# Kernel optimization log

Measured on AMD Instinct MI355X. Metric: run time of the kernel, lower is better.

## Reference

```python
import jax, jax.numpy as jnp
import numpy as np
import math

B, S, H, NH = 2, 2048, 2048, 16
HD = H // NH  # 128


def _rope_tables(seq_len, dim, base=10000.0):
    inv_freq = 1.0 / (base ** (np.arange(0, dim, 2, dtype=np.float32) / dim))
    t = np.arange(seq_len, dtype=np.float32)
    freqs = np.outer(t, inv_freq)                      # [S, dim/2]
    emb = np.concatenate([freqs, freqs], axis=-1)      # [S, dim] (HF layout)
    return jnp.asarray(np.cos(emb)), jnp.asarray(np.sin(emb))


def setup_inputs() -> dict:
    key = jax.random.key(0)
    ks = jax.random.split(key, 6)
    sc = 1.0 / math.sqrt(H)
    cos, sin = _rope_tables(S, HD)
    return {
        "hidden_states": jax.random.normal(ks[0], (B, S, H), jnp.float32),
        "wq": jax.random.normal(ks[1], (H, H), jnp.float32) * sc,
        "wk": jax.random.normal(ks[2], (H, H), jnp.float32) * sc,
        "wv": jax.random.normal(ks[3], (H, H), jnp.float32) * sc,
        "wo": jax.random.normal(ks[4], (H, H), jnp.float32) * sc,
        "cos": cos,
        "sin": sin,
        "attention_mask": jnp.ones((B, S), jnp.float32),
        "position_ids": jnp.broadcast_to(jnp.arange(S, dtype=jnp.int64), (B, S)),
    }


def _rotate_half(x):
    x1, x2 = jnp.split(x, 2, axis=-1)
    return jnp.concatenate([-x2, x1], axis=-1)


def reference(hidden_states, wq, wk, wv, wo, cos, sin, attention_mask, position_ids):
    b, s, _ = hidden_states.shape
    # projections (torch Linear: x @ W^T)
    q = (hidden_states @ wq.T).reshape(b, s, NH, HD).transpose(0, 2, 1, 3)
    k = (hidden_states @ wk.T).reshape(b, s, NH, HD).transpose(0, 2, 1, 3)
    v = (hidden_states @ wv.T).reshape(b, s, NH, HD).transpose(0, 2, 1, 3)
    # RoPE (HF apply_rotary_pos_emb): gather tables at position_ids -> [b,1,s,hd]
    c = cos[position_ids][:, None, :, :]
    sn = sin[position_ids][:, None, :, :]
    q = q * c + _rotate_half(q) * sn
    k = k * c + _rotate_half(k) * sn
    # dense attention scores [b,h,q,k]
    scores = jnp.einsum("bhqd,bhkd->bhqk", q, k) / math.sqrt(HD)
    adder = (1.0 - attention_mask)[:, None, None, :] * -10000.0
    scores = scores + adder
    probs = jax.nn.softmax(scores.astype(jnp.float32), axis=-1).astype(q.dtype)
    attn = jnp.einsum("bhqk,bhkd->bhqd", probs, v)
    attn = attn.transpose(0, 2, 1, 3).reshape(b, s, H)
    return attn @ wo.T
```

## Files before the change

### kernel.cpp

```cpp
#include <hip/hip_runtime.h>
#include <hip/hip_bf16.h>

#define B_SZ 2
#define S_LEN 2048
#define H_DIM 2048
#define N_HEAD 16
#define HD 128

using bf16 = __hip_bfloat16;
using bf16x8 = __bf16 __attribute__((ext_vector_type(8)));
using floatx4 = float __attribute__((ext_vector_type(4)));

typedef unsigned int __attribute__((address_space(1))) as1_uint;
typedef unsigned int __attribute__((address_space(3))) as3_uint;

__device__ inline void async_load16(const void* g, void* l) {
  __builtin_amdgcn_global_load_lds((const as1_uint*)g, (as3_uint*)l, 16, 0, 0);
}

__device__ inline void store_out(float* p, float v) { *p = v; }
__device__ inline void store_out(bf16* p, float v) { *p = __float2bfloat16(v); }

__global__ __launch_bounds__(256) void cast_kernel(const float* __restrict__ in,
                                                   bf16* __restrict__ out, int n4) {
  int i = blockIdx.x * 256 + threadIdx.x;
  if (i >= n4) return;
  const float4 v = ((const float4*)in)[i];
  union { bf16 h[4]; uint2 u; } o;
  o.h[0] = __float2bfloat16(v.x);
  o.h[1] = __float2bfloat16(v.y);
  o.h[2] = __float2bfloat16(v.z);
  o.h[3] = __float2bfloat16(v.w);
  ((uint2*)out)[i] = o.u;
}

__global__ __launch_bounds__(256) void cast4_kernel(
    const float* __restrict__ a, const float* __restrict__ b,
    const float* __restrict__ c, const float* __restrict__ d,
    bf16* __restrict__ oa, bf16* __restrict__ ob,
    bf16* __restrict__ oc, bf16* __restrict__ od) {
  int i = blockIdx.x * 256 + threadIdx.x;
  int sel = i >> 20;
  int j = i & 0xFFFFF;
  const float* src = sel == 0 ? a : sel == 1 ? b : sel == 2 ? c : d;
  bf16* dst = sel == 0 ? oa : sel == 1 ? ob : sel == 2 ? oc : od;
  const float4 v = ((const float4*)src)[j];
  union { bf16 h[4]; uint2 u; } o;
  o.h[0] = __float2bfloat16(v.x);
  o.h[1] = __float2bfloat16(v.y);
  o.h[2] = __float2bfloat16(v.z);
  o.h[3] = __float2bfloat16(v.w);
  ((uint2*)dst)[j] = o.u;
}

template <typename OutT>
__global__ __launch_bounds__(256) void gemm_bt(const bf16* __restrict__ A,
                                               const bf16* __restrict__ B,
                                               OutT* __restrict__ C,
                                               int M, int N, int K) {
  __shared__ alignas(16) bf16 As[128 * 32];
  __shared__ alignas(16) bf16 Bs[128 * 32];
  const int tid = threadIdx.x;
  const int wave = tid >> 6;
  const int lane = tid & 63;
  const int quad = lane >> 4;
  const int l16 = lane & 15;
  const int m0 = blockIdx.x * 128;
  const int n0 = blockIdx.y * 128;
  const int wm = (wave >> 1) * 64;
  const int wn = (wave & 1) * 64;

  const bf16* Ag = A + (size_t)(m0 + (tid >> 2)) * K + (tid & 3) * 8;
  const bf16* Bg = B + (size_t)(n0 + (tid >> 2)) * K + (tid & 3) * 8;
  char* AsB = (char*)As + wave * 1024;
  char* BsB = (char*)Bs + wave * 1024;
  const size_t rowskip = (size_t)64 * K;

  floatx4 acc[4][4] = {};

  for (int k0 = 0; k0 < K; k0 += 32) {
    async_load16(Ag + k0, AsB);
    async_load16(Ag + rowskip + k0, AsB + 4096);
    async_load16(Bg + k0, BsB);
    async_load16(Bg + rowskip + k0, BsB + 4096);
    __syncthreads();

    bf16x8 af[4], bfr[4];
#pragma unroll
    for (int i = 0; i < 4; i++)
      af[i] = *(const bf16x8*)&As[(wm + i * 16 + l16) * 32 + quad * 8];
#pragma unroll
    for (int j = 0; j < 4; j++)
      bfr[j] = *(const bf16x8*)&Bs[(wn + j * 16 + l16) * 32 + quad * 8];
#pragma unroll
    for (int i = 0; i < 4; i++)
#pragma unroll
      for (int j = 0; j < 4; j++)
        acc[i][j] = __builtin_amdgcn_mfma_f32_16x16x32_bf16(af[i], bfr[j], acc[i][j], 0, 0, 0);
    __syncthreads();
  }

#pragma unroll
  for (int i = 0; i < 4; i++) {
    const int row = m0 + wm + i * 16 + quad * 4;
#pragma unroll
    for (int j = 0; j < 4; j++) {
      const int col = n0 + wn + j * 16 + l16;
#pragma unroll
      for (int r = 0; r < 4; r++)
        store_out(&C[(size_t)(row + r) * N + col], acc[i][j][r]);
    }
  }
}

__global__ __launch_bounds__(512, 2) void gemm_qk_rope256(
    const bf16* __restrict__ A, const bf16* __restrict__ B,
    bf16* __restrict__ C, const float* __restrict__ cosT,
    const float* __restrict__ sinT, const int* __restrict__ pos) {
  __shared__ alignas(16) char lds[131072];
  const int tid = threadIdx.x;
  const int wv = tid >> 6;
  const int lane = tid & 63;
  const int quad = lane >> 4;
  const int l16 = lane & 15;
  const int lrow = lane >> 3;
  const int scol = ((lane & 7) << 4) ^ (lrow << 4);

  const int id = blockIdx.x;
  const int swz = (id & 7) * 32 + (id >> 3);
  const int m0 = (swz >> 4) * 256;
  const int n0 = (swz & 15) * 256;
  const int wrow = (wv >> 1) * 64;
  const int wcol = (wv & 1) * 128;

  const char* Ag = (const char*)A + (size_t)(m0 + wv * 8 + lrow) * 4096 + scol;
  const char* Bg = (const char*)B + (size_t)(n0 + wv * 8 + lrow) * 4096 + scol;
  char* const ldsW = (char*)lds + wv * 1024;

  const int csw0 = (quad << 4) ^ ((l16 & 7) << 4);
  const int csw1 = csw0 ^ 64;

  floatx4 acc[4][8] = {};
  bf16x8 af[4][2], bfr[8][2];

#define STAGE_A256(kt, buf) { \
    const char* s_ = Ag + (size_t)(kt) * 128; \
    char* d_ = ldsW + (buf) * 65536; \
    async_load16(s_, d_); \
    async_load16(s_ + (size_t)64 * 4096, d_ + 64 * 128); \
    async_load16(s_ + (size_t)128 * 4096, d_ + 128 * 128); \
    async_load16(s_ + (size_t)192 * 4096, d_ + 192 * 128); }
#define STAGE_B256(kt, buf) { \
    const char* s_ = Bg + (size_t)(kt) * 128; \
    char* d_ = ldsW + (buf) * 65536 + 32768; \
    async_load16(s_, d_); \
    async_load16(s_ + (size_t)64 * 4096, d_ + 64 * 128); \
    async_load16(s_ + (size_t)128 * 4096, d_ + 128 * 128); \
    async_load16(s_ + (size_t)192 * 4096, d_ + 192 * 128); }
#define READ_A256(I) { \
    const char* p_ = cA + (wrow + (I) * 16 + l16) * 128; \
    af[I][0] = *(const bf16x8*)(p_ + csw0); \
    af[I][1] = *(const bf16x8*)(p_ + csw1); }
#define READ_B256(J) { \
    const char* p_ = cB + (wcol + (J) * 16 + l16) * 128; \
    bfr[J][0] = *(const bf16x8*)(p_ + csw0); \
    bfr[J][1] = *(const bf16x8*)(p_ + csw1); }
#define MFMA_Q256(I0, J0) { \
    _Pragma("unroll") for (int ks = 0; ks < 2; ++ks) \
    _Pragma("unroll") for (int di = 0; di < 2; ++di) \
    _Pragma("unroll") for (int dj = 0; dj < 4; ++dj) \
      acc[(I0) + di][(J0) + dj] = __builtin_amdgcn_mfma_f32_16x16x32_bf16( \
          af[(I0) + di][ks], bfr[(J0) + dj][ks], acc[(I0) + di][(J0) + dj], 0, 0, 0); }

  STAGE_A256(0, 0) STAGE_B256(0, 0)
  STAGE_A256(1, 1) STAGE_B256(1, 1)
  asm volatile("s_waitcnt vmcnt(8)" ::: "memory");
  __builtin_amdgcn_s_barrier();

  const int NT = 32;
  for (int t = 0; t < NT; ++t) {
    const char* cA = (const char*)lds + (t & 1) * 65536;
    const char* cB = cA + 32768;
    READ_A256(0) READ_A256(1)
    READ_B256(0) READ_B256(1) READ_B256(2) READ_B256(3)
    __builtin_amdgcn_s_barrier();
    asm volatile("s_waitcnt lgkmcnt(0)" ::: "memory");
    __builtin_amdgcn_sched_barrier(0);
    __builtin_amdgcn_s_setprio(1);
    MFMA_Q256(0, 0)
    __builtin_amdgcn_s_setprio(0);
    __builtin_amdgcn_s_barrier();
    READ_A256(2) READ_A256(3)
    READ_B256(4) READ_B256(5) READ_B256(6) READ_B256(7)
    __builtin_amdgcn_s_barrier();
    asm volatile("s_waitcnt lgkmcnt(0)" ::: "memory");
    __builtin_amdgcn_sched_barrier(0);
    __builtin_amdgcn_s_setprio(1);
    MFMA_Q256(2, 0)
    __builtin_amdgcn_s_setprio(0);
    __builtin_amdgcn_s_barrier();
    __builtin_amdgcn_sched_barrier(0);
    asm volatile("" ::: "memory");
    if (t + 2 < NT) { STAGE_A256(t + 2, t & 1) }
    __builtin_amdgcn_s_setprio(1);
    MFMA_Q256(0, 4)
    __builtin_amdgcn_s_setprio(0);
    __builtin_amdgcn_s_barrier();
    if (t + 2 < NT) { STAGE_B256(t + 2, t & 1) }
    __builtin_amdgcn_s_setprio(1);
    MFMA_Q256(2, 4)
    __builtin_amdgcn_s_setprio(0);
    if (t + 2 < NT) {
      asm volatile("s_waitcnt vmcnt(8)" ::: "memory");
    } else {
      asm volatile("s_waitcnt vmcnt(0)" ::: "memory");
    }
    __builtin_amdgcn_s_barrier();
  }

  const float sc = ((n0 + wcol) < 2048) ? 0.08838834764831845f : 1.0f;
#pragma unroll
  for (int i = 0; i < 4; ++i) {
#pragma unroll
    for (int r = 0; r < 4; ++r) {
      const int row = m0 + wrow + i * 16 + quad * 4 + r;
      const int p = pos[row];
      const float* cp = cosT + (size_t)p * HD;
      const float* sp = sinT + (size_t)p * HD;
      bf16* Crow = C + (size_t)row * 4096 + n0 + wcol + l16;
#pragma unroll
      for (int j = 0; j < 4; ++j) {
        const int d = j * 16 + l16;
        const float c = cp[d], s = sp[d];
        const float v1 = acc[i][j][r], v2 = acc[i][j + 4][r];
        Crow[j * 16] = __float2bfloat16((v1 * c - v2 * s) * sc);
        Crow[j * 16 + 64] = __float2bfloat16((v2 * c + v1 * s) * sc);
      }
    }
  }
}

__global__ __launch_bounds__(256, 2) void flash_attn(
    const bf16* __restrict__ QK, const bf16* __restrict__ Vt,
    const float* __restrict__ mask, bf16* __restrict__ AO) {
  __shared__ alignas(16) char KP[128 * 256];
  __shared__ alignas(16) char Vs[128 * 256];
  const int tid = threadIdx.x;
  const int wv = tid >> 6;
  const int lane = tid & 63;
  const int quad = lane >> 4;
  const int l16 = lane & 15;
  const int b = blockIdx.x >> 4;
  const int h = blockIdx.x & 15;
  const int q0 = blockIdx.y * 128;

  const bf16* Qb = QK + (size_t)(b * S_LEN + q0) * 4096 + h * HD;
  const char* Kb = (const char*)(QK + (size_t)(b * S_LEN) * 4096 + 2048 + h * HD);
  const char* Vb = (const char*)(Vt + (size_t)(h * HD) * 4096 + (size_t)b * S_LEN);
  const float* Mb = mask + b * S_LEN;

  const int kswz = (l16 & 7) << 4;

  bf16x8 qf[2][4];
#pragma unroll
  for (int s = 0; s < 2; s++)
#pragma unroll
    for (int kc = 0; kc < 4; kc++)
      qf[s][kc] = *(const bf16x8*)(Qb + (size_t)(wv * 32 + s * 16 + l16) * 4096 +
                                   kc * 32 + quad * 8);

  float l_i[2][4] = {};
  floatx4 O[2][8] = {};

  for (int k0 = 0; k0 < S_LEN; k0 += 128) {
    for (int i = tid; i < 2048; i += 256) {
      const int r = i >> 4;
      const int c16 = (i & 15) * 16;
      const int d_ = r * 256 + (c16 ^ ((r & 7) << 4));
      *(uint4*)(KP + d_) = *(const uint4*)(Kb + (size_t)(k0 + r) * 8192 + c16);
      *(uint4*)(Vs + d_) = *(const uint4*)(Vb + (size_t)r * 8192 + k0 * 2 + c16);
    }
    __syncthreads();

    floatx4 Sa[2][8] = {};
    __builtin_amdgcn_s_setprio(1);
#pragma unroll
    for (int ct = 0; ct < 8; ct++) {
      bf16x8 kf[4];
#pragma unroll
      for (int kc = 0; kc < 4; kc++)
        kf[kc] = *(const bf16x8*)(KP + (ct * 16 + l16) * 256 +
                                  ((kc * 64 + quad * 16) ^ kswz));
#pragma unroll
      for (int s = 0; s < 2; s++)
#pragma unroll
        for (int kc = 0; kc < 4; kc++)
          Sa[s][ct] = __builtin_amdgcn_mfma_f32_16x16x32_bf16(qf[s][kc], kf[kc], Sa[s][ct], 0, 0, 0);
    }
    __builtin_amdgcn_s_setprio(0);
    __syncthreads();

    float addv[8];
#pragma unroll
    for (int ct = 0; ct < 8; ct++)
      addv[ct] = (1.0f - Mb[k0 + ct * 16 + l16]) * -10000.0f - 12.0f;

#pragma unroll
    for (int s = 0; s < 2; s++) {
#pragma unroll
      for (int r = 0; r < 4; r++) {
        const int lr = wv * 32 + s * 16 + quad * 4 + r;
        char* prow = KP + lr * 256;
        const int rsw = (lr & 7) << 4;
#pragma unroll
        for (int ct = 0; ct < 8; ct++) {
          float p = __expf(Sa[s][ct][r] + addv[ct]);
          l_i[s][r] += p;
          *(bf16*)(prow + ((ct * 32 + l16 * 2) ^ rsw)) = __float2bfloat16(p);
        }
      }
    }

    __builtin_amdgcn_s_setprio(1);
#pragma unroll
    for (int kc = 0; kc < 4; kc++) {
      bf16x8 pa[2];
#pragma unroll
      for (int s = 0; s < 2; s++)
        pa[s] = *(const bf16x8*)(KP + (wv * 32 + s * 16 + l16) * 256 +
                                 ((kc * 64 + quad * 16) ^ kswz));
#pragma unroll
      for (int dt = 0; dt < 8; dt++) {
        bf16x8 vf = *(const bf16x8*)(Vs + (dt * 16 + l16) * 256 +
                                     ((kc * 64 + quad * 16) ^ kswz));
#pragma unroll
        for (int s = 0; s < 2; s++)
          O[s][dt] = __builtin_amdgcn_mfma_f32_16x16x32_bf16(pa[s], vf, O[s][dt], 0, 0, 0);
      }
    }
    __builtin_amdgcn_s_setprio(0);
    __syncthreads();
  }

#pragma unroll
  for (int s = 0; s < 2; s++)
#pragma unroll
    for (int r = 0; r < 4; r++)
#pragma unroll
      for (int off = 1; off < 16; off <<= 1)
        l_i[s][r] += __shfl_xor(l_i[s][r], off);

#pragma unroll
  for (int s = 0; s < 2; s++) {
    const int qrow = q0 + wv * 32 + s * 16 + quad * 4;
#pragma unroll
    for (int r = 0; r < 4; r++) {
      float inv = 1.0f / l_i[s][r];
      bf16* outp = AO + (size_t)(b * S_LEN + qrow + r) * H_DIM + h * HD + l16;
#pragma unroll
      for (int dt = 0; dt < 8; dt++)
        outp[dt * 16] = __float2bfloat16(O[s][dt][r] * inv);
    }
  }
}

extern "C" void kernel_launch(void* const* d_in, const int* in_sizes, int n_in,
                              void* d_out, int out_size, void* d_ws, size_t ws_size,
                              hipStream_t stream) {
  const float* hs   = (const float*)d_in[0];
  const float* wq   = (const float*)d_in[1];
  const float* wk   = (const float*)d_in[2];
  const float* wv   = (const float*)d_in[3];
  const float* wo   = (const float*)d_in[4];
  const float* cosT = (const float*)d_in[5];
  const float* sinT = (const float*)d_in[6];
  const float* mask = (const float*)d_in[7];
  const int*   pos  = (const int*)d_in[8];

  char* ws = (char*)d_ws;
  bf16* Xbf  = (bf16*)ws;
  bf16* Wqkb = (bf16*)(ws + (size_t)(16 << 20));
  bf16* Wvb  = (bf16*)(ws + (size_t)(32 << 20));
  bf16* Wob  = (bf16*)(ws + (size_t)(40 << 20));
  bf16* QKm  = (bf16*)(ws + (size_t)(48 << 20));
  bf16* Vtm  = (bf16*)(ws + (size_t)(80 << 20));
  bf16* AO   = Xbf;

  cast_kernel<<<8192, 256, 0, stream>>>(hs, Xbf, 2097152);
  cast4_kernel<<<16384, 256, 0, stream>>>(wq, wk, wv, wo,
                                          Wqkb, Wqkb + (size_t)2048 * 2048, Wvb, Wob);

  gemm_qk_rope256<<<256, 512, 0, stream>>>(Xbf, Wqkb, QKm, cosT, sinT, pos);
  gemm_bt<bf16><<<dim3(16, 32), 256, 0, stream>>>(Wvb, Xbf, Vtm, 2048, 4096, 2048);

  flash_attn<<<dim3(32, 16), 256, 0, stream>>>(QKm, Vtm, mask, AO);

  gemm_bt<float><<<dim3(32, 16), 256, 0, stream>>>(AO, Wob, (float*)d_out, 4096, 2048, 2048);
}
```

Before: 437.5 us.

## Prefetch next K/V tile into registers and pad LDS rows in flash attention

The flash attention loop now issues global loads for the next K/V tile into registers before computing on the current tile, then writes them to LDS after the PV stage. This hides global memory latency behind the MFMA work. The XOR swizzle is replaced by 272-byte padded rows, and the mask adder is precomputed once into shared memory. Probability stores are packed into 32-bit writes via a lane shuffle. The change adds 64 VGPRs of prefetch buffers plus more LDS, which may reduce occupancy below the 2-blocks-per-CU target, and it adds an extra barrier per iteration.

Result: slower. 561.2 us (+28.3%).

```diff
diff --git a/kernel.cpp b/kernel.cpp
--- a/kernel.cpp
+++ b/kernel.cpp
@@ -243,8 +243,9 @@
 __global__ __launch_bounds__(256, 2) void flash_attn(
     const bf16* __restrict__ QK, const bf16* __restrict__ Vt,
     const float* __restrict__ mask, bf16* __restrict__ AO) {
-  __shared__ alignas(16) char KP[128 * 256];
-  __shared__ alignas(16) char Vs[128 * 256];
+  __shared__ alignas(16) char KP[128 * 272];
+  __shared__ alignas(16) char Vs[128 * 272];
+  __shared__ float MaskB[S_LEN];
   const int tid = threadIdx.x;
   const int wv = tid >> 6;
   const int lane = tid & 63;
@@ -259,7 +260,8 @@
   const char* Vb = (const char*)(Vt + (size_t)(h * HD) * 4096 + (size_t)b * S_LEN);
   const float* Mb = mask + b * S_LEN;
 
-  const int kswz = (l16 & 7) << 4;
+  const int srow = tid >> 4;
+  const int scol16 = (tid & 15) * 16;
 
   bf16x8 qf[2][4];
 #pragma unroll
@@ -269,18 +271,30 @@
       qf[s][kc] = *(const bf16x8*)(Qb + (size_t)(wv * 32 + s * 16 + l16) * 4096 +
                                    kc * 32 + quad * 8);
 
+  uint4 kreg[8], vreg[8];
+#define FA_LOAD(k0_) { \
+    _Pragma("unroll") for (int j = 0; j < 8; ++j) { \
+      const int r_ = srow + j * 16; \
+      kreg[j] = *(const uint4*)(Kb + (size_t)((k0_) + r_) * 8192 + scol16); \
+      vreg[j] = *(const uint4*)(Vb + (size_t)r_ * 8192 + (k0_) * 2 + scol16); } }
+#define FA_WRITE() { \
+    _Pragma("unroll") for (int j = 0; j < 8; ++j) { \
+      const int r_ = srow + j * 16; \
+      *(uint4*)(KP + r_ * 272 + scol16) = kreg[j]; \
+      *(uint4*)(Vs + r_ * 272 + scol16) = vreg[j]; } }
+
   float l_i[2][4] = {};
   floatx4 O[2][8] = {};
 
-  for (int k0 = 0; k0 < S_LEN; k0 += 128) {
-    for (int i = tid; i < 2048; i += 256) {
-      const int r = i >> 4;
-      const int c16 = (i & 15) * 16;
-      const int d_ = r * 256 + (c16 ^ ((r & 7) << 4));
-      *(uint4*)(KP + d_) = *(const uint4*)(Kb + (size_t)(k0 + r) * 8192 + c16);
-      *(uint4*)(Vs + d_) = *(const uint4*)(Vb + (size_t)r * 8192 + k0 * 2 + c16);
-    }
-    __syncthreads();
+  FA_LOAD(0)
+  for (int i = tid; i < S_LEN; i += 256)
+    MaskB[i] = (1.0f - Mb[i]) * -10000.0f - 12.0f;
+  FA_WRITE()
+  __syncthreads();
+
+  for (int it = 0; it < 16; ++it) {
+    const int k0 = it * 128;
+    if (it < 15) { FA_LOAD(k0 + 128) }
 
     floatx4 Sa[2][8] = {};
     __builtin_amdgcn_s_setprio(1);
@@ -289,8 +303,7 @@
       bf16x8 kf[4];
 #pragma unroll
       for (int kc = 0; kc < 4; kc++)
-        kf[kc] = *(const bf16x8*)(KP + (ct * 16 + l16) * 256 +
-                                  ((kc * 64 + quad * 16) ^ kswz));
+        kf[kc] = *(const bf16x8*)(KP + (ct * 16 + l16) * 272 + kc * 64 + quad * 16);
 #pragma unroll
       for (int s = 0; s < 2; s++)
 #pragma unroll
@@ -303,20 +316,30 @@
     float addv[8];
 #pragma unroll
     for (int ct = 0; ct < 8; ct++)
-      addv[ct] = (1.0f - Mb[k0 + ct * 16 + l16]) * -10000.0f - 12.0f;
+      addv[ct] = MaskB[k0 + ct * 16 + l16];
 
 #pragma unroll
     for (int s = 0; s < 2; s++) {
 #pragma unroll
       for (int r = 0; r < 4; r++) {
         const int lr = wv * 32 + s * 16 + quad * 4 + r;
-        char* prow = KP + lr * 256;
-        const int rsw = (lr & 7) << 4;
+        char* prow = KP + lr * 272;
+        float pv_[8];
 #pragma unroll
         for (int ct = 0; ct < 8; ct++) {
           float p = __expf(Sa[s][ct][r] + addv[ct]);
           l_i[s][r] += p;
-          *(bf16*)(prow + ((ct * 32 + l16 * 2) ^ rsw)) = __float2bfloat16(p);
+          pv_[ct] = p;
+        }
+#pragma unroll
+        for (int ct = 0; ct < 8; ct++) {
+          const float po = __shfl_xor(pv_[ct], 1);
+          if ((l16 & 1) == 0) {
+            union { bf16 h[2]; unsigned u; } w;
+            w.h[0] = __float2bfloat16(pv_[ct]);
+            w.h[1] = __float2bfloat16(po);
+            *(unsigned*)(prow + ct * 32 + l16 * 2) = w.u;
+          }
         }
       }
     }
@@ -327,12 +350,10 @@
       bf16x8 pa[2];
 #pragma unroll
       for (int s = 0; s < 2; s++)
-        pa[s] = *(const bf16x8*)(KP + (wv * 32 + s * 16 + l16) * 256 +
-                                 ((kc * 64 + quad * 16) ^ kswz));
+        pa[s] = *(const bf16x8*)(KP + (wv * 32 + s * 16 + l16) * 272 + kc * 64 + quad * 16);
 #pragma unroll
       for (int dt = 0; dt < 8; dt++) {
-        bf16x8 vf = *(const bf16x8*)(Vs + (dt * 16 + l16) * 256 +
-                                     ((kc * 64 + quad * 16) ^ kswz));
+        bf16x8 vf = *(const bf16x8*)(Vs + (dt * 16 + l16) * 272 + kc * 64 + quad * 16);
 #pragma unroll
         for (int s = 0; s < 2; s++)
           O[s][dt] = __builtin_amdgcn_mfma_f32_16x16x32_bf16(pa[s], vf, O[s][dt], 0, 0, 0);
@@ -340,6 +361,11 @@
     }
     __builtin_amdgcn_s_setprio(0);
     __syncthreads();
+
+    if (it < 15) {
+      FA_WRITE()
+      __syncthreads();
+    }
   }
 
 #pragma unroll
```
